# Optimization experiments

Hardware: AMD Instinct MI355X
Metric: run time of the kernel (lower is better)

The kernel has to match this reference:

```python
import jax, jax.numpy as jnp
import numpy as np
from jax import lax

KD, KH, KW = 9, 9, 9  # box-filter window (matches torch ones([1,1,9,9,9]))


def _box_sum(x):
    """Sum over a 9x9x9 window with SAME (zero) padding, via separable 1D convs.
    x: [B, 1, D, H, W]. Mathematically identical to conv3d with an all-ones
    9x9x9 kernel, but O(3k) instead of O(k^3) work per voxel.
    """
    dn = ('NCDHW', 'OIDHW', 'NCDHW')
    dt = x.dtype
    kd = jnp.ones((1, 1, KD, 1, 1), dt)
    kh = jnp.ones((1, 1, 1, KH, 1), dt)
    kw = jnp.ones((1, 1, 1, 1, KW), dt)
    pd, ph, pw = (KD - 1) // 2, (KH - 1) // 2, (KW - 1) // 2
    x = lax.conv_general_dilated(x, kd, (1, 1, 1), [(pd, pd), (0, 0), (0, 0)], dimension_numbers=dn)
    x = lax.conv_general_dilated(x, kh, (1, 1, 1), [(0, 0), (ph, ph), (0, 0)], dimension_numbers=dn)
    x = lax.conv_general_dilated(x, kw, (1, 1, 1), [(0, 0), (0, 0), (pw, pw)], dimension_numbers=dn)
    return x


def setup_inputs() -> dict:
    key = jax.random.key(0)
    k1, k2 = jax.random.split(key)
    shape = (2, 1, 160, 192, 160)  # [B, C=1, D, H, W]
    return {
        'input': jax.random.normal(k1, shape, dtype=jnp.float32),
        'target': jax.random.normal(k2, shape, dtype=jnp.float32),
    }


def reference(input, target):
    ksize = jnp.asarray(KD * KH * KW, input.dtype)
    I_sum = _box_sum(input)
    T_sum = _box_sum(target)
    II_sum = _box_sum(input * input)
    TT_sum = _box_sum(target * target)
    IT_sum = _box_sum(input * target)

    Ihat = I_sum / ksize
    That = T_sum / ksize
    cross = IT_sum - Ihat * T_sum - That * I_sum + That * Ihat * ksize
    T_var = TT_sum - 2 * That * T_sum + That * That * ksize
    I_var = II_sum - 2 * Ihat * I_sum + Ihat * Ihat * ksize
    cc = cross * cross / (T_var * I_var + 1e-5)
    return -1.0 * jnp.mean(cc)
```

## Files before the change

kernel.cpp:

```cpp
#include <hip/hip_runtime.h>

#define DIM_W 160
#define DIM_H 192
#define DIM_D 160
#define DIM_B 2

constexpr int TW = 16;
constexpr int TH = 32;
constexpr int CH = 19;
constexpr int NCH = 9;
constexpr int RH = TH + 8;
constexpr float INV_K = 1.0f / 729.0f;
constexpr double NTOT = 9830400.0;

typedef unsigned int u32;
typedef __attribute__((address_space(1))) const u32 gu32;
typedef __attribute__((address_space(3))) u32 lu32;

__global__ void init_kernel(float* out, float* ws) {
    out[0] = 0.0f;
    ws[0] = 0.0f; ws[1] = 0.0f; ws[2] = 0.0f; ws[3] = 0.0f;
}

__device__ __forceinline__ int clampD(int s) {
    return s < 0 ? 0 : (s > DIM_D - 1 ? DIM_D - 1 : s);
}

__global__ __launch_bounds__(256)
void lncc3d_kernel(const float* __restrict__ I,
                   const float* __restrict__ T,
                   const float* __restrict__ zsrc,
                   float* __restrict__ out)
{
    __shared__ __align__(16) float sR[2][2][RH][32];
    __shared__ __align__(16) float4 wA[RH][16];
    __shared__ __align__(16) float  wB[16][44];
    __shared__ float red[4];

    const int tid  = threadIdx.x;
    const int lane = tid & 63;
    const int wid  = tid >> 6;
    const int wo   = tid & 15;
    const int hb   = (tid >> 4) << 1;

    const int bw = blockIdx.x, bh = blockIdx.y, bz = blockIdx.z;
    const int b  = bz / NCH;
    const int c  = bz - b * NCH;
    const int w0 = bw * TW, h0 = bh * TH, d0 = c * CH;
    const int dEnd = min(d0 + CH, DIM_D);

    const int plane = DIM_H * DIM_W;
    const int fld  = wid >> 1;
    const int kodd = wid & 1;
    const int nck  = kodd ? 2 : 3;
    const float* Fb = (fld ? T : I) + (size_t)b * DIM_D * plane;

    int boff[3], crw[3];
#pragma unroll
    for (int i = 0; i < 3; ++i) {
        const int ck  = kodd ? (2 * i + 1) : (2 * i);
        const int row = 8 * ck + (lane >> 3);
        const int pf4 = lane & 7;
        const int lf4 = (pf4 - 2 * row) & 7;
        const int gh  = h0 - 4 + row;
        const int gw  = w0 - 8 + (lf4 << 2);
        crw[i]  = 8 * ck;
        boff[i] = (i < nck && gh >= 0 && gh < DIM_H && gw >= 0 && gw <= DIM_W - 4)
                  ? (gh * DIM_W + gw) : -1;
    }

    auto issue = [&](int sc, int buf) {
        const float* Fs = Fb + (size_t)sc * plane;
#pragma unroll
        for (int i = 0; i < 3; ++i) {
            if (i < nck) {
                const float* gp = (boff[i] >= 0) ? (Fs + boff[i]) : zsrc;
                __builtin_amdgcn_global_load_lds((gu32*)gp, (lu32*)&sR[buf][fld][crw[i]][0],
                                                 16, 0, 0);
            }
        }
    };

    float rgI[2][9], rgT[2][9], rgII[2][9], rgTT[2][9], rgIT[2][9];
    float rnI[2], rnT[2], rnII[2], rnTT[2], rnIT[2];
#pragma unroll
    for (int p = 0; p < 2; ++p) {
        rnI[p] = rnT[p] = rnII[p] = rnTT[p] = rnIT[p] = 0.0f;
#pragma unroll
        for (int q = 0; q < 9; ++q) {
            rgI[p][q] = rgT[p][q] = rgII[p][q] = rgTT[p][q] = rgIT[p][q] = 0.0f;
        }
    }
    float acc = 0.0f;

    const int sStart = d0 - 4;
    int cur = 0;

    issue(clampD(sStart), 0);
    issue(clampD(sStart + 1), 1);
    if (kodd) { asm volatile("s_waitcnt vmcnt(2)" ::: "memory"); }
    else      { asm volatile("s_waitcnt vmcnt(3)" ::: "memory"); }
    __builtin_amdgcn_s_barrier();

    for (int t = 0; t < 3; ++t) {
        const int t9 = t * 9;
#pragma unroll
        for (int j = 0; j < 9; ++j) {
            const int s  = sStart + t9 + j;
            const bool vs = (s >= 0) && (s < DIM_D);

            if (vs && tid < 160) {
                const int r = tid >> 2;
                const int g = tid & 3;
                const float* rIp = &sR[cur][0][r][0];
                const float* rTp = &sR[cur][1][r][0];
                const int q0 = ((g + 1 + 2 * r) & 7) << 2;
                const int q1 = ((g + 2 + 2 * r) & 7) << 2;
                const int q2 = ((g + 3 + 2 * r) & 7) << 2;
                const float4 ia  = *(const float4*)(rIp + q0);
                const float4 ib4 = *(const float4*)(rIp + q1);
                const float4 ic4 = *(const float4*)(rIp + q2);
                const float4 ta  = *(const float4*)(rTp + q0);
                const float4 tb4 = *(const float4*)(rTp + q1);
                const float4 tc4 = *(const float4*)(rTp + q2);
                const float iv[12] = {ia.x, ia.y, ia.z, ia.w, ib4.x, ib4.y, ib4.z, ib4.w,
                                      ic4.x, ic4.y, ic4.z, ic4.w};
                const float tv[12] = {ta.x, ta.y, ta.z, ta.w, tb4.x, tb4.y, tb4.z, tb4.w,
                                      tc4.x, tc4.y, tc4.z, tc4.w};
                float aI = 0.f, aT = 0.f, aII = 0.f, aTT = 0.f, aIT = 0.f;
#pragma unroll
                for (int k = 0; k < 9; ++k) {
                    aI += iv[k]; aT += tv[k];
                    aII = fmaf(iv[k], iv[k], aII);
                    aTT = fmaf(tv[k], tv[k], aTT);
                    aIT = fmaf(iv[k], tv[k], aIT);
                }
                const int c0 = g << 2;
                wA[r][(c0 + r) & 15] = make_float4(aI, aT, aII, aTT);
                wB[c0][r] = aIT;
#pragma unroll
                for (int q = 1; q < 4; ++q) {
                    const float ni = iv[8 + q], oi = iv[q - 1];
                    const float nt = tv[8 + q], ot = tv[q - 1];
                    aI += ni - oi; aT += nt - ot;
                    aII = fmaf(ni, ni, fmaf(oi, -oi, aII));
                    aTT = fmaf(nt, nt, fmaf(ot, -ot, aTT));
                    aIT = fmaf(ni, nt, fmaf(oi, -ot, aIT));
                    wA[r][(c0 + q + r) & 15] = make_float4(aI, aT, aII, aTT);
                    wB[c0 + q][r] = aIT;
                }
            }
            asm volatile("s_waitcnt lgkmcnt(0)" ::: "memory");
            __builtin_amdgcn_s_barrier();

            issue(clampD(s + 2), cur);

            float s2I0, s2T0, s2II0, s2TT0, s2IT0, s2I1, s2T1, s2II1, s2TT1, s2IT1;
            if (vs) {
                const float4 A0 = wA[hb][(wo + hb) & 15];
                float sx = A0.x, sy = A0.y, szv = A0.z, swv = A0.w;
#pragma unroll
                for (int k = 1; k < 9; ++k) {
                    const float4 Ak = wA[hb + k][(wo + hb + k) & 15];
                    sx += Ak.x; sy += Ak.y; szv += Ak.z; swv += Ak.w;
                }
                const float4 A9 = wA[hb + 9][(wo + hb + 9) & 15];
                const float2 B0 = *(const float2*)&wB[wo][hb];
                const float2 B1 = *(const float2*)&wB[wo][hb + 2];
                const float2 B2 = *(const float2*)&wB[wo][hb + 4];
                const float2 B3 = *(const float2*)&wB[wo][hb + 6];
                const float2 B4 = *(const float2*)&wB[wo][hb + 8];
                const float sbv = B0.x + B0.y + B1.x + B1.y + B2.x + B2.y
                                + B3.x + B3.y + B4.x;
                s2I0 = sx; s2T0 = sy; s2II0 = szv; s2TT0 = swv; s2IT0 = sbv;
                s2I1  = sx  - A0.x + A9.x;
                s2T1  = sy  - A0.y + A9.y;
                s2II1 = szv - A0.z + A9.z;
                s2TT1 = swv - A0.w + A9.w;
                s2IT1 = sbv - B0.x + B4.y;
            } else {
                s2I0 = s2T0 = s2II0 = s2TT0 = s2IT0 = 0.f;
                s2I1 = s2T1 = s2II1 = s2TT1 = s2IT1 = 0.f;
            }

            rnI[0]  += s2I0  - rgI[0][j];  rgI[0][j]  = s2I0;
            rnT[0]  += s2T0  - rgT[0][j];  rgT[0][j]  = s2T0;
            rnII[0] += s2II0 - rgII[0][j]; rgII[0][j] = s2II0;
            rnTT[0] += s2TT0 - rgTT[0][j]; rgTT[0][j] = s2TT0;
            rnIT[0] += s2IT0 - rgIT[0][j]; rgIT[0][j] = s2IT0;
            rnI[1]  += s2I1  - rgI[1][j];  rgI[1][j]  = s2I1;
            rnT[1]  += s2T1  - rgT[1][j];  rgT[1][j]  = s2T1;
            rnII[1] += s2II1 - rgII[1][j]; rgII[1][j] = s2II1;
            rnTT[1] += s2TT1 - rgTT[1][j]; rgTT[1][j] = s2TT1;
            rnIT[1] += s2IT1 - rgIT[1][j]; rgIT[1][j] = s2IT1;

            if ((s >= d0 + 4) && ((s - 4) < dEnd)) {
                float cr, vv, tvv;
                cr  = rnIT[0] - rnI[0] * rnT[0] * INV_K;
                vv  = rnII[0] - rnI[0] * rnI[0] * INV_K;
                tvv = rnTT[0] - rnT[0] * rnT[0] * INV_K;
                acc += cr * cr * __builtin_amdgcn_rcpf(fmaf(tvv, vv, 1e-5f));
                cr  = rnIT[1] - rnI[1] * rnT[1] * INV_K;
                vv  = rnII[1] - rnI[1] * rnI[1] * INV_K;
                tvv = rnTT[1] - rnT[1] * rnT[1] * INV_K;
                acc += cr * cr * __builtin_amdgcn_rcpf(fmaf(tvv, vv, 1e-5f));
            }

            asm volatile("s_waitcnt lgkmcnt(0)" ::: "memory");
            if (kodd) { asm volatile("s_waitcnt vmcnt(2)" ::: "memory"); }
            else      { asm volatile("s_waitcnt vmcnt(3)" ::: "memory"); }
            __builtin_amdgcn_s_barrier();
            cur ^= 1;
        }
    }

#pragma unroll
    for (int off = 32; off > 0; off >>= 1) acc += __shfl_down(acc, off, 64);
    if (lane == 0) red[wid] = acc;
    __syncthreads();
    if (tid == 0) {
        const float bs = red[0] + red[1] + red[2] + red[3];
        atomicAdd(out, bs * (float)(-1.0 / NTOT));
    }
}

extern "C" void kernel_launch(void* const* d_in, const int* in_sizes, int n_in,
                              void* d_out, int out_size, void* d_ws, size_t ws_size,
                              hipStream_t stream) {
    const float* I = (const float*)d_in[0];
    const float* T = (const float*)d_in[1];
    float* out = (float*)d_out;
    float* ws  = (float*)d_ws;

    init_kernel<<<dim3(1), dim3(1), 0, stream>>>(out, ws);

    dim3 grid(DIM_W / TW, DIM_H / TH, DIM_B * NCH);
    dim3 block(256);
    lncc3d_kernel<<<grid, block, 0, stream>>>(I, T, ws, out);
}
```

Before: 82.44 us.

## Lengthen depth chunks and pack halo rows into 24-float LDS rows

The depth chunk per block grows from 19 to 28 slices (6 chunks instead of 9), so the 8-slice depth halo that each block warms up on is amortised over more output slices. The LDS staging layout also changes: each row now holds only the 24 needed floats (a 4-column halo) instead of 32 with an 8-column halo and swizzle. This cuts the loads per slice per wave from 3 to 2 and makes the wait counts uniform. The trade-off is fewer blocks in the grid, which lowers parallelism and wave-level load balance, and possible LDS bank conflicts from the unswizzled 24-float stride.

```diff
diff --git a/kernel.cpp b/kernel.cpp
--- a/kernel.cpp
+++ b/kernel.cpp
@@ -7,9 +7,10 @@
 
 constexpr int TW = 16;
 constexpr int TH = 32;
-constexpr int CH = 19;
-constexpr int NCH = 9;
+constexpr int CH = 28;
+constexpr int NCH = 6;
 constexpr int RH = TH + 8;
+constexpr int RWDS = 24;
 constexpr float INV_K = 1.0f / 729.0f;
 constexpr double NTOT = 9830400.0;
 
@@ -32,9 +33,9 @@
                    const float* __restrict__ zsrc,
                    float* __restrict__ out)
 {
-    __shared__ __align__(16) float sR[2][2][RH][32];
+    __shared__ __align__(16) float sR[2][2][1024];
     __shared__ __align__(16) float4 wA[RH][16];
-    __shared__ __align__(16) float  wB[16][44];
+    __shared__ __align__(16) float  wB[16][42];
     __shared__ float red[4];
 
     const int tid  = threadIdx.x;
@@ -50,34 +51,31 @@
     const int dEnd = min(d0 + CH, DIM_D);
 
     const int plane = DIM_H * DIM_W;
-    const int fld  = wid >> 1;
-    const int kodd = wid & 1;
-    const int nck  = kodd ? 2 : 3;
+    const int fld = wid >> 1;
+    const int khi = wid & 1;
     const float* Fb = (fld ? T : I) + (size_t)b * DIM_D * plane;
 
-    int boff[3], crw[3];
-#pragma unroll
-    for (int i = 0; i < 3; ++i) {
-        const int ck  = kodd ? (2 * i + 1) : (2 * i);
-        const int row = 8 * ck + (lane >> 3);
-        const int pf4 = lane & 7;
-        const int lf4 = (pf4 - 2 * row) & 7;
+    int boff[2], ldof[2];
+#pragma unroll
+    for (int i = 0; i < 2; ++i) {
+        const int ck  = (khi << 1) | i;
+        const int s16 = ck * 64 + lane;
+        const int row = s16 / 6;
+        const int q   = s16 - row * 6;
         const int gh  = h0 - 4 + row;
-        const int gw  = w0 - 8 + (lf4 << 2);
-        crw[i]  = 8 * ck;
-        boff[i] = (i < nck && gh >= 0 && gh < DIM_H && gw >= 0 && gw <= DIM_W - 4)
+        const int gw  = w0 - 4 + (q << 2);
+        ldof[i] = ck << 8;
+        boff[i] = (row < RH && gh >= 0 && gh < DIM_H && gw >= 0 && gw <= DIM_W - 4)
                   ? (gh * DIM_W + gw) : -1;
     }
 
     auto issue = [&](int sc, int buf) {
         const float* Fs = Fb + (size_t)sc * plane;
 #pragma unroll
-        for (int i = 0; i < 3; ++i) {
-            if (i < nck) {
-                const float* gp = (boff[i] >= 0) ? (Fs + boff[i]) : zsrc;
-                __builtin_amdgcn_global_load_lds((gu32*)gp, (lu32*)&sR[buf][fld][crw[i]][0],
-                                                 16, 0, 0);
-            }
+        for (int i = 0; i < 2; ++i) {
+            const float* gp = (boff[i] >= 0) ? (Fs + boff[i]) : zsrc;
+            __builtin_amdgcn_global_load_lds((gu32*)gp, (lu32*)&sR[buf][fld][ldof[i]],
+                                             16, 0, 0);
         }
     };
 
@@ -98,11 +96,10 @@
 
     issue(clampD(sStart), 0);
     issue(clampD(sStart + 1), 1);
-    if (kodd) { asm volatile("s_waitcnt vmcnt(2)" ::: "memory"); }
-    else      { asm volatile("s_waitcnt vmcnt(3)" ::: "memory"); }
+    asm volatile("s_waitcnt vmcnt(2)" ::: "memory");
     __builtin_amdgcn_s_barrier();
 
-    for (int t = 0; t < 3; ++t) {
+    for (int t = 0; t < 4; ++t) {
         const int t9 = t * 9;
 #pragma unroll
         for (int j = 0; j < 9; ++j) {
@@ -110,19 +107,17 @@
             const bool vs = (s >= 0) && (s < DIM_D);
 
             if (vs && tid < 160) {
-                const int r = tid >> 2;
-                const int g = tid & 3;
-                const float* rIp = &sR[cur][0][r][0];
-                const float* rTp = &sR[cur][1][r][0];
-                const int q0 = ((g + 1 + 2 * r) & 7) << 2;
-                const int q1 = ((g + 2 + 2 * r) & 7) << 2;
-                const int q2 = ((g + 3 + 2 * r) & 7) << 2;
-                const float4 ia  = *(const float4*)(rIp + q0);
-                const float4 ib4 = *(const float4*)(rIp + q1);
-                const float4 ic4 = *(const float4*)(rIp + q2);
-                const float4 ta  = *(const float4*)(rTp + q0);
-                const float4 tb4 = *(const float4*)(rTp + q1);
-                const float4 tc4 = *(const float4*)(rTp + q2);
+                const int r  = tid >> 2;
+                const int g  = tid & 3;
+                const int c0 = g << 2;
+                const float* rIp = &sR[cur][0][r * RWDS];
+                const float* rTp = &sR[cur][1][r * RWDS];
+                const float4 ia  = *(const float4*)(rIp + c0);
+                const float4 ib4 = *(const float4*)(rIp + c0 + 4);
+                const float4 ic4 = *(const float4*)(rIp + c0 + 8);
+                const float4 ta  = *(const float4*)(rTp + c0);
+                const float4 tb4 = *(const float4*)(rTp + c0 + 4);
+                const float4 tc4 = *(const float4*)(rTp + c0 + 8);
                 const float iv[12] = {ia.x, ia.y, ia.z, ia.w, ib4.x, ib4.y, ib4.z, ib4.w,
                                       ic4.x, ic4.y, ic4.z, ic4.w};
                 const float tv[12] = {ta.x, ta.y, ta.z, ta.w, tb4.x, tb4.y, tb4.z, tb4.w,
@@ -135,7 +130,6 @@
                     aTT = fmaf(tv[k], tv[k], aTT);
                     aIT = fmaf(iv[k], tv[k], aIT);
                 }
-                const int c0 = g << 2;
                 wA[r][(c0 + r) & 15] = make_float4(aI, aT, aII, aTT);
                 wB[c0][r] = aIT;
 #pragma unroll
@@ -207,8 +201,7 @@
             }
 
             asm volatile("s_waitcnt lgkmcnt(0)" ::: "memory");
-            if (kodd) { asm volatile("s_waitcnt vmcnt(2)" ::: "memory"); }
-            else      { asm volatile("s_waitcnt vmcnt(3)" ::: "memory"); }
+            asm volatile("s_waitcnt vmcnt(2)" ::: "memory");
             __builtin_amdgcn_s_barrier();
             cur ^= 1;
         }
```

Result: slower. 86.33 us (+4.7%).
